# Kernel optimization log

Measured on AMD Instinct MI355X. Metric: run time of the kernel, lower is better.

Reference implementation:

```python
import jax, jax.numpy as jnp
import numpy as np

NEG_INF = -1e9
ALPHA = 0.2  # LeakyReLU slope


def gat_layer(x, adj, W, a_src, a_dst):
    # x: (N, F), adj: (N, N) bool, W: (F, H, D), a_src/a_dst: (H, D)
    h = jnp.einsum('nf,fhd->nhd', x, W)                 # (N, H, D)
    es = jnp.einsum('nhd,hd->nh', h, a_src)             # score from target node i
    ed = jnp.einsum('nhd,hd->nh', h, a_dst)             # score from neighbor j
    e = jax.nn.leaky_relu(es[:, None, :] + ed[None, :, :], ALPHA)  # (N, N, H)
    e = jnp.where(adj[:, :, None], e, NEG_INF)
    attn = jax.nn.softmax(e, axis=1)                    # softmax over neighbors j
    out = jnp.einsum('ijh,jhd->ihd', attn, h)           # (N, H, D)
    N, H, D = out.shape
    return out.reshape(N, H * D)                        # concat heads


def setup_inputs() -> dict:
    key = jax.random.key(0)
    ks = jax.random.split(key, 8)
    N, F, H1, D1, C = 4096, 512, 8, 8, 16
    node_matrix = jax.random.normal(ks[0], (N, F), dtype=jnp.float32)
    adj = jax.random.bernoulli(ks[1], 0.005, (N, N))
    adj = jnp.logical_or(adj, jnp.eye(N, dtype=bool))   # self-loops
    s1 = 1.0 / np.sqrt(F)
    s2 = 1.0 / np.sqrt(H1 * D1)
    return {
        'node_matrix': node_matrix,
        'adj_matrix': adj,
        'W1': jax.random.normal(ks[2], (F, H1, D1), dtype=jnp.float32) * s1,
        'a1_src': jax.random.normal(ks[3], (H1, D1), dtype=jnp.float32) * s1,
        'a1_dst': jax.random.normal(ks[4], (H1, D1), dtype=jnp.float32) * s1,
        'W2': jax.random.normal(ks[5], (H1 * D1, 1, C), dtype=jnp.float32) * s2,
        'a2_src': jax.random.normal(ks[6], (1, C), dtype=jnp.float32) * s2,
        'a2_dst': jax.random.normal(ks[7], (1, C), dtype=jnp.float32) * s2,
    }


def reference(node_matrix, adj_matrix, W1, a1_src, a1_dst, W2, a2_src, a2_dst):
    # dropout layers are identity in eval mode
    z1 = gat_layer(node_matrix, adj_matrix, W1, a1_src, a1_dst)  # (N, 64)
    a1 = jax.nn.elu(z1)
    z2 = gat_layer(a1, adj_matrix, W2, a2_src, a2_dst)           # (N, num_classes)
    return z2
```

## Files before the change

### kernel.cpp

```cpp
#include <hip/hip_runtime.h>

#define N_NODES 4096
#define F_IN    512
#define NH1     8
#define F1      64
#define C2      16
#define MAXDEG  128

__device__ __forceinline__ float wave_sum(float v) {
    for (int o = 32; o >= 1; o >>= 1) v += __shfl_xor(v, o, 64);
    return v;
}

__global__ void detect_width_kernel(const unsigned char* __restrict__ adj,
                                    int* __restrict__ flag) {
    __shared__ unsigned int cnts[4];
    __shared__ unsigned int mxv;
    int t = threadIdx.x;
    if (t < 4) cnts[t] = 0u;
    if (t == 0) mxv = 0u;
    __syncthreads();
    unsigned int c0 = 0, c1 = 0, c2 = 0, c3 = 0, m = 0;
    const unsigned int* p = (const unsigned int*)(adj) + t * 64;
    for (int i = 0; i < 64; ++i) {
        unsigned int v = p[i];
        unsigned int b0 = v & 0xffu, b1 = (v >> 8) & 0xffu;
        unsigned int b2 = (v >> 16) & 0xffu, b3 = (v >> 24) & 0xffu;
        if (b0) { c0++; m = m > b0 ? m : b0; }
        if (b1) { c1++; m = m > b1 ? m : b1; }
        if (b2) { c2++; m = m > b2 ? m : b2; }
        if (b3) { c3++; m = m > b3 ? m : b3; }
    }
    atomicAdd(&cnts[0], c0); atomicAdd(&cnts[1], c1);
    atomicAdd(&cnts[2], c2); atomicAdd(&cnts[3], c3);
    atomicMax(&mxv, m);
    __syncthreads();
    if (t == 0) {
        int w;
        if (cnts[1] + cnts[2] + cnts[3] == 0u)      w = 4;
        else if (cnts[0] == 0u && cnts[1] == 0u)    w = 4;
        else if (cnts[0] == 0u && cnts[2] == 0u)    w = 2;
        else if (mxv <= 1u)                          w = 1;
        else                                         w = 2;
        *flag = w;
    }
}

__global__ __launch_bounds__(256) void frontend_kernel(
        const unsigned char* __restrict__ adj, const int* __restrict__ flag,
        unsigned short* __restrict__ neigh, int* __restrict__ deg,
        const float* __restrict__ x, const float* __restrict__ W1,
        const float* __restrict__ asrc, const float* __restrict__ adst,
        float* __restrict__ h1, float* __restrict__ es, float* __restrict__ ed) {
    __shared__ __align__(16) char smem[24576];
    const int t = threadIdx.x;

    if (blockIdx.x < N_NODES) {
        int* cnt = (int*)smem;
        const int row = blockIdx.x;
        if (t == 0) *cnt = 0;
        __syncthreads();
        const int w = *flag;
        unsigned short* outp = neigh + (size_t)row * MAXDEG;
        if (w == 1) {
            const uint4* p = (const uint4*)(adj + (size_t)row * N_NODES);
            uint4 v = p[t];
            if (v.x | v.y | v.z | v.w) {
                unsigned int wd[4] = {v.x, v.y, v.z, v.w};
                int base = t * 16;
                for (int q = 0; q < 4; ++q) {
                    unsigned int word = wd[q];
                    for (int bb = 0; bb < 4; ++bb) {
                        if ((word >> (8 * bb)) & 0xffu) {
                            int pos = atomicAdd(cnt, 1);
                            if (pos < MAXDEG) outp[pos] = (unsigned short)(base + q * 4 + bb);
                        }
                    }
                }
            }
        } else if (w == 2) {
            const uint4* p = (const uint4*)(adj + (size_t)row * N_NODES * 2);
            uint4 v[2];
            #pragma unroll
            for (int i = 0; i < 2; ++i) v[i] = p[t + i * 256];
            #pragma unroll
            for (int i = 0; i < 2; ++i) {
                if ((v[i].x | v[i].y | v[i].z | v[i].w) == 0u) continue;
                unsigned int wd[4] = {v[i].x, v[i].y, v[i].z, v[i].w};
                int base = (t + i * 256) * 8;
                for (int q = 0; q < 4; ++q) {
                    unsigned int word = wd[q];
                    if (word & 0xffffu) {
                        int pos = atomicAdd(cnt, 1);
                        if (pos < MAXDEG) outp[pos] = (unsigned short)(base + q * 2);
                    }
                    if (word >> 16) {
                        int pos = atomicAdd(cnt, 1);
                        if (pos < MAXDEG) outp[pos] = (unsigned short)(base + q * 2 + 1);
                    }
                }
            }
        } else {
            const uint4* p = (const uint4*)(adj + (size_t)row * N_NODES * 4);
            uint4 v[4];
            #pragma unroll
            for (int i = 0; i < 4; ++i) v[i] = p[t + i * 256];
            #pragma unroll
            for (int i = 0; i < 4; ++i) {
                if ((v[i].x | v[i].y | v[i].z | v[i].w) == 0u) continue;
                unsigned int wd[4] = {v[i].x, v[i].y, v[i].z, v[i].w};
                int base = (t + i * 256) * 4;
                for (int q = 0; q < 4; ++q) {
                    if (wd[q]) {
                        int pos = atomicAdd(cnt, 1);
                        if (pos < MAXDEG) outp[pos] = (unsigned short)(base + q);
                    }
                }
            }
        }
        __syncthreads();
        if (t == 0) deg[row] = min(*cnt, MAXDEG);
    } else {
        float* xs = (float*)smem;
        float* wt = (float*)(smem + 8192);
        const int row0 = (blockIdx.x - N_NODES) * 4;
        const float4* src = (const float4*)(x + (size_t)row0 * F_IN);
        float4* dst = (float4*)xs;
        for (int i = t; i < 4 * F_IN / 4; i += 256) dst[i] = src[i];
        const int c = t & 63;
        const int r = t >> 6;
        const float4* w1v = (const float4*)W1;
        float4* wtv = (float4*)wt;
        float a = 0.f;
        for (int k0 = 0; k0 < F_IN; k0 += 64) {
            __syncthreads();
            #pragma unroll
            for (int i = 0; i < 4; ++i)
                wtv[t + i * 256] = w1v[k0 * 16 + t + i * 256];
            __syncthreads();
            const float4* xr = (const float4*)&xs[r * F_IN + k0];
            #pragma unroll
            for (int kk = 0; kk < 64; kk += 4) {
                float4 xv = xr[kk >> 2];
                float w0 = wt[(kk + 0) * 64 + c];
                float w1 = wt[(kk + 1) * 64 + c];
                float w2 = wt[(kk + 2) * 64 + c];
                float w3 = wt[(kk + 3) * 64 + c];
                a += xv.x * w0 + xv.y * w1 + xv.z * w2 + xv.w * w3;
            }
        }
        const int n = row0 + r;
        h1[(size_t)n * F1 + c] = a;
        float s = a * asrc[c];
        float d = a * adst[c];
        s += __shfl_xor(s, 1); s += __shfl_xor(s, 2); s += __shfl_xor(s, 4);
        d += __shfl_xor(d, 1); d += __shfl_xor(d, 2); d += __shfl_xor(d, 4);
        if ((c & 7) == 0) {
            es[n * NH1 + (c >> 3)] = s;
            ed[n * NH1 + (c >> 3)] = d;
        }
    }
}

__global__ __launch_bounds__(256) void attn1_kernel(
        const unsigned short* __restrict__ neigh, const int* __restrict__ deg,
        const float* __restrict__ h1, const float* __restrict__ es,
        const float* __restrict__ ed, const float* __restrict__ W2,
        const float* __restrict__ a2s, const float* __restrict__ a2d,
        float* __restrict__ h2, float* __restrict__ es2, float* __restrict__ ed2) {
    __shared__ unsigned short listA[4 * MAXDEG];
    __shared__ float arowA[4 * 64];
    __shared__ float pbufA[4 * 576];
    const int t = threadIdx.x;
    const int wv = t >> 6;
    const int l = t & 63;
    const int i = blockIdx.x * 4 + wv;
    unsigned short* list = listA + wv * MAXDEG;
    float* arow = arowA + wv * 64;
    float* pw   = pbufA + wv * 576;
    const int hq = l >> 3;

    const int K = deg[i];
    const unsigned short* lst = neigh + (size_t)i * MAXDEG;
    for (int j = l; j < MAXDEG; j += 64) list[j] = (j < K) ? lst[j] : (unsigned short)0;
    __syncthreads();

    float plsum[NH1], esi[NH1];
    #pragma unroll
    for (int h = 0; h < NH1; ++h) plsum[h] = 0.f;
    #pragma unroll
    for (int h = 0; h < NH1; ++h) esi[h] = es[i * NH1 + h];
    float acc = 0.f;

    for (int t0 = 0; t0 < MAXDEG; t0 += 64) {
        const int tc = min(64, K - t0);
        if (tc > 0) {
            const bool valid = l < tc;
            const int j = valid ? (int)list[t0 + l] : 0;
            #pragma unroll
            for (int h = 0; h < NH1; ++h) {
                float v = esi[h] + ed[j * NH1 + h];
                v = (v >= 0.f) ? v : 0.2f * v;
                float p = valid ? __expf(v) : 0.f;
                plsum[h] += p;
                pw[l * 9 + h] = p;
            }
        }
        __syncthreads();
        if (tc > 0) {
            const int tcPad = (tc + 7) & ~7;
            for (int u = 0; u < tcPad; u += 8) {
                #pragma unroll
                for (int vv = 0; vv < 8; ++vv) {
                    int jn = (int)list[t0 + u + vv];
                    acc += pw[(u + vv) * 9 + hq] * h1[(size_t)jn * F1 + l];
                }
            }
        }
        __syncthreads();
    }
    float lsum[NH1];
    #pragma unroll
    for (int h = 0; h < NH1; ++h) lsum[h] = wave_sum(plsum[h]);
    float o = acc / lsum[hq];
    float a1v = (o > 0.f) ? o : (__expf(o) - 1.f);

    arow[l] = a1v;
    __syncthreads();
    const int cc = l & 15;
    const int kg = l >> 4;
    float hacc = 0.f;
    #pragma unroll
    for (int k = 0; k < 16; ++k)
        hacc += arow[kg * 16 + k] * W2[(kg * 16 + k) * C2 + cc];
    hacc += __shfl_xor(hacc, 16);
    hacc += __shfl_xor(hacc, 32);
    if (l < C2) h2[(size_t)i * C2 + l] = hacc;
    float s2 = hacc * a2s[cc];
    float d2 = hacc * a2d[cc];
    s2 += __shfl_xor(s2, 1); s2 += __shfl_xor(s2, 2);
    s2 += __shfl_xor(s2, 4); s2 += __shfl_xor(s2, 8);
    d2 += __shfl_xor(d2, 1); d2 += __shfl_xor(d2, 2);
    d2 += __shfl_xor(d2, 4); d2 += __shfl_xor(d2, 8);
    if (l == 0) { es2[i] = s2; ed2[i] = d2; }
}

__global__ __launch_bounds__(256) void attn2_kernel(
        const unsigned short* __restrict__ neigh, const int* __restrict__ deg,
        const float* __restrict__ h2, const float* __restrict__ es2,
        const float* __restrict__ ed2, float* __restrict__ out) {
    __shared__ unsigned short listA[4 * MAXDEG];
    __shared__ float pbufA[4 * 64];
    const int t = threadIdx.x;
    const int wv = t >> 6;
    const int l = t & 63;
    const int i = blockIdx.x * 4 + wv;
    unsigned short* list = listA + wv * MAXDEG;
    float* pb = pbufA + wv * 64;
    const int c = l & 15;
    const int g = l >> 4;

    const int K = deg[i];
    const unsigned short* lst = neigh + (size_t)i * MAXDEG;
    for (int j = l; j < MAXDEG; j += 64) list[j] = (j < K) ? lst[j] : (unsigned short)0;
    __syncthreads();

    float plsum = 0.f, acc = 0.f;
    const float esi = es2[i];
    for (int t0 = 0; t0 < MAXDEG; t0 += 64) {
        const int tc = min(64, K - t0);
        if (tc > 0) {
            const bool valid = l < tc;
            const int j = valid ? (int)list[t0 + l] : 0;
            float v = esi + ed2[j];
            v = (v >= 0.f) ? v : 0.2f * v;
            float p = valid ? __expf(v) : 0.f;
            plsum += p;
            pb[l] = p;
        }
        __syncthreads();
        if (tc > 0) {
            const int tcPad = (tc + 3) & ~3;
            for (int u = g; u < tcPad; u += 4) {
                int jn = (int)list[t0 + u];
                acc += pb[u] * h2[(size_t)jn * C2 + c];
            }
        }
        __syncthreads();
    }
    float lsum = wave_sum(plsum);
    acc += __shfl_xor(acc, 16);
    acc += __shfl_xor(acc, 32);
    if (l < C2) out[(size_t)i * C2 + l] = acc / lsum;
}

extern "C" void kernel_launch(void* const* d_in, const int* in_sizes, int n_in,
                              void* d_out, int out_size, void* d_ws, size_t ws_size,
                              hipStream_t stream) {
    const float* x           = (const float*)d_in[0];
    const unsigned char* adj = (const unsigned char*)d_in[1];
    const float* W1          = (const float*)d_in[2];
    const float* a1src       = (const float*)d_in[3];
    const float* a1dst       = (const float*)d_in[4];
    const float* W2          = (const float*)d_in[5];
    const float* a2src       = (const float*)d_in[6];
    const float* a2dst       = (const float*)d_in[7];
    float* out = (float*)d_out;

    char* ws = (char*)d_ws;
    size_t off = 0;
    int* flag = (int*)(ws + off);                 off += 256;
    unsigned short* neigh = (unsigned short*)(ws + off);
    off += (size_t)N_NODES * MAXDEG * 2;
    int* deg = (int*)(ws + off);                  off += (size_t)N_NODES * 4;
    float* h1 = (float*)(ws + off);               off += (size_t)N_NODES * F1 * 4;
    float* es1 = (float*)(ws + off);              off += (size_t)N_NODES * NH1 * 4;
    float* ed1 = (float*)(ws + off);              off += (size_t)N_NODES * NH1 * 4;
    float* h2 = (float*)(ws + off);               off += (size_t)N_NODES * C2 * 4;
    float* es2 = (float*)(ws + off);              off += (size_t)N_NODES * 4;
    float* ed2 = (float*)(ws + off);              off += (size_t)N_NODES * 4;

    hipLaunchKernelGGL(detect_width_kernel, dim3(1), dim3(256), 0, stream, adj, flag);
    hipLaunchKernelGGL(frontend_kernel, dim3(N_NODES + N_NODES / 4), dim3(256), 0, stream,
                       adj, flag, neigh, deg, x, W1, a1src, a1dst, h1, es1, ed1);
    hipLaunchKernelGGL(attn1_kernel, dim3(N_NODES / 4), dim3(256), 0, stream,
                       neigh, deg, h1, es1, ed1, W2, a2src, a2dst, h2, es2, ed2);
    hipLaunchKernelGGL(attn2_kernel, dim3(N_NODES / 4), dim3(256), 0, stream,
                       neigh, deg, h2, es2, ed2, out);
}
```

Measured before the change: 158.4 us.

## Restructure frontend GEMM with 8-row double-buffered tiles and per-wave adjacency scan

The W1 projection now computes 8 rows per block, reusing each loaded W1 tile across twice as many rows and prefetching the next tile into a second shared buffer. Adjacency scanning moves from one row per 256-thread block to one row per wavefront, with each lane loading several uint4s. The attention kernels swap block-wide syncthreads for wave barriers, since each wave works on its own data, and their neighbor loops now stop at the real degree. The detect kernel reads uint4 vectors. Together these aim to cut W1 reloads, block count and sync overhead, at the cost of more registers and LDS per block.

```diff
diff --git a/kernel.cpp b/kernel.cpp
--- a/kernel.cpp
+++ b/kernel.cpp
@@ -6,6 +6,9 @@
 #define F1      64
 #define C2      16
 #define MAXDEG  128
+
+#define GEMM_BLKS (N_NODES / 8)
+#define SCAN_BLKS (N_NODES / 4)
 
 __device__ __forceinline__ float wave_sum(float v) {
     for (int o = 32; o >= 1; o >>= 1) v += __shfl_xor(v, o, 64);
@@ -21,15 +24,21 @@
     if (t == 0) mxv = 0u;
     __syncthreads();
     unsigned int c0 = 0, c1 = 0, c2 = 0, c3 = 0, m = 0;
-    const unsigned int* p = (const unsigned int*)(adj) + t * 64;
-    for (int i = 0; i < 64; ++i) {
-        unsigned int v = p[i];
-        unsigned int b0 = v & 0xffu, b1 = (v >> 8) & 0xffu;
-        unsigned int b2 = (v >> 16) & 0xffu, b3 = (v >> 24) & 0xffu;
-        if (b0) { c0++; m = m > b0 ? m : b0; }
-        if (b1) { c1++; m = m > b1 ? m : b1; }
-        if (b2) { c2++; m = m > b2 ? m : b2; }
-        if (b3) { c3++; m = m > b3 ? m : b3; }
+    const uint4* p = (const uint4*)(adj) + t * 16;
+    #pragma unroll
+    for (int i = 0; i < 16; ++i) {
+        uint4 q = p[i];
+        unsigned int wd[4] = {q.x, q.y, q.z, q.w};
+        #pragma unroll
+        for (int k = 0; k < 4; ++k) {
+            unsigned int v = wd[k];
+            unsigned int b0 = v & 0xffu, b1 = (v >> 8) & 0xffu;
+            unsigned int b2 = (v >> 16) & 0xffu, b3 = (v >> 24) & 0xffu;
+            if (b0) { c0++; m = m > b0 ? m : b0; }
+            if (b1) { c1++; m = m > b1 ? m : b1; }
+            if (b2) { c2++; m = m > b2 ? m : b2; }
+            if (b3) { c3++; m = m > b3 ? m : b3; }
+        }
     }
     atomicAdd(&cnts[0], c0); atomicAdd(&cnts[1], c1);
     atomicAdd(&cnts[2], c2); atomicAdd(&cnts[3], c3);
@@ -52,22 +61,94 @@
         const float* __restrict__ x, const float* __restrict__ W1,
         const float* __restrict__ asrc, const float* __restrict__ adst,
         float* __restrict__ h1, float* __restrict__ es, float* __restrict__ ed) {
-    __shared__ __align__(16) char smem[24576];
+    __shared__ __align__(16) float smem[4096 + 2 * 4096];
+    __shared__ int scnt[4];
     const int t = threadIdx.x;
-
-    if (blockIdx.x < N_NODES) {
-        int* cnt = (int*)smem;
-        const int row = blockIdx.x;
-        if (t == 0) *cnt = 0;
-        __syncthreads();
+    const int wv = t >> 6;
+    const int l = t & 63;
+
+    if (blockIdx.x < GEMM_BLKS) {
+        float* xs  = smem;
+        float* wt0 = smem + 4096;
+        float* wt1 = smem + 8192;
+        const int row0 = blockIdx.x * 8;
+
+        {
+            const float4* src = (const float4*)(x + (size_t)row0 * F_IN);
+            float4* dst = (float4*)xs;
+            #pragma unroll
+            for (int i = 0; i < 4; ++i) dst[t + i * 256] = src[t + i * 256];
+        }
+        const float4* w1v = (const float4*)W1;
+        {
+            float4* d = (float4*)wt0;
+            #pragma unroll
+            for (int i = 0; i < 4; ++i) d[t + i * 256] = w1v[t + i * 256];
+        }
+
+        const int c = t & 63;
+        const int rq = t >> 6;
+        float a0 = 0.f, a1 = 0.f;
+        float* wcur = wt0;
+        float* wnxt = wt1;
+        for (int tile = 0; tile < 8; ++tile) {
+            __syncthreads();
+            float4 pf0, pf1, pf2, pf3;
+            if (tile < 7) {
+                const float4* s = w1v + (size_t)(tile + 1) * 1024;
+                pf0 = s[t]; pf1 = s[t + 256]; pf2 = s[t + 512]; pf3 = s[t + 768];
+            }
+            const float4* xr0 = (const float4*)&xs[rq * F_IN + tile * 64];
+            const float4* xr1 = (const float4*)&xs[(rq + 4) * F_IN + tile * 64];
+            #pragma unroll
+            for (int kk = 0; kk < 64; kk += 4) {
+                float4 x0 = xr0[kk >> 2];
+                float4 x1 = xr1[kk >> 2];
+                float w0 = wcur[(kk + 0) * 64 + c];
+                float w1 = wcur[(kk + 1) * 64 + c];
+                float w2 = wcur[(kk + 2) * 64 + c];
+                float w3 = wcur[(kk + 3) * 64 + c];
+                a0 += x0.x * w0 + x0.y * w1 + x0.z * w2 + x0.w * w3;
+                a1 += x1.x * w0 + x1.y * w1 + x1.z * w2 + x1.w * w3;
+            }
+            if (tile < 7) {
+                float4* d = (float4*)wnxt;
+                d[t] = pf0; d[t + 256] = pf1; d[t + 512] = pf2; d[t + 768] = pf3;
+            }
+            float* tmp = wcur; wcur = wnxt; wnxt = tmp;
+        }
+
+        const int n0 = row0 + rq;
+        h1[(size_t)n0 * F1 + c] = a0;
+        h1[(size_t)(n0 + 4) * F1 + c] = a1;
+        float s0 = a0 * asrc[c], d0 = a0 * adst[c];
+        float s1 = a1 * asrc[c], d1 = a1 * adst[c];
+        s0 += __shfl_xor(s0, 1); s0 += __shfl_xor(s0, 2); s0 += __shfl_xor(s0, 4);
+        d0 += __shfl_xor(d0, 1); d0 += __shfl_xor(d0, 2); d0 += __shfl_xor(d0, 4);
+        s1 += __shfl_xor(s1, 1); s1 += __shfl_xor(s1, 2); s1 += __shfl_xor(s1, 4);
+        d1 += __shfl_xor(d1, 1); d1 += __shfl_xor(d1, 2); d1 += __shfl_xor(d1, 4);
+        if ((c & 7) == 0) {
+            es[n0 * NH1 + (c >> 3)] = s0;
+            ed[n0 * NH1 + (c >> 3)] = d0;
+            es[(n0 + 4) * NH1 + (c >> 3)] = s1;
+            ed[(n0 + 4) * NH1 + (c >> 3)] = d1;
+        }
+    } else {
+        const int row = (blockIdx.x - GEMM_BLKS) * 4 + wv;
+        int* cnt = scnt + wv;
+        if (l == 0) *cnt = 0;
         const int w = *flag;
         unsigned short* outp = neigh + (size_t)row * MAXDEG;
         if (w == 1) {
             const uint4* p = (const uint4*)(adj + (size_t)row * N_NODES);
-            uint4 v = p[t];
-            if (v.x | v.y | v.z | v.w) {
-                unsigned int wd[4] = {v.x, v.y, v.z, v.w};
-                int base = t * 16;
+            uint4 v[4];
+            #pragma unroll
+            for (int i = 0; i < 4; ++i) v[i] = p[l + 64 * i];
+            #pragma unroll
+            for (int i = 0; i < 4; ++i) {
+                if ((v[i].x | v[i].y | v[i].z | v[i].w) == 0u) continue;
+                unsigned int wd[4] = {v[i].x, v[i].y, v[i].z, v[i].w};
+                int base = (l + 64 * i) * 16;
                 for (int q = 0; q < 4; ++q) {
                     unsigned int word = wd[q];
                     for (int bb = 0; bb < 4; ++bb) {
@@ -80,14 +161,14 @@
             }
         } else if (w == 2) {
             const uint4* p = (const uint4*)(adj + (size_t)row * N_NODES * 2);
-            uint4 v[2];
-            #pragma unroll
-            for (int i = 0; i < 2; ++i) v[i] = p[t + i * 256];
-            #pragma unroll
-            for (int i = 0; i < 2; ++i) {
+            uint4 v[8];
+            #pragma unroll
+            for (int i = 0; i < 8; ++i) v[i] = p[l + 64 * i];
+            #pragma unroll
+            for (int i = 0; i < 8; ++i) {
                 if ((v[i].x | v[i].y | v[i].z | v[i].w) == 0u) continue;
                 unsigned int wd[4] = {v[i].x, v[i].y, v[i].z, v[i].w};
-                int base = (t + i * 256) * 8;
+                int base = (l + 64 * i) * 8;
                 for (int q = 0; q < 4; ++q) {
                     unsigned int word = wd[q];
                     if (word & 0xffffu) {
@@ -102,63 +183,26 @@
             }
         } else {
             const uint4* p = (const uint4*)(adj + (size_t)row * N_NODES * 4);
-            uint4 v[4];
-            #pragma unroll
-            for (int i = 0; i < 4; ++i) v[i] = p[t + i * 256];
-            #pragma unroll
-            for (int i = 0; i < 4; ++i) {
-                if ((v[i].x | v[i].y | v[i].z | v[i].w) == 0u) continue;
-                unsigned int wd[4] = {v[i].x, v[i].y, v[i].z, v[i].w};
-                int base = (t + i * 256) * 4;
-                for (int q = 0; q < 4; ++q) {
-                    if (wd[q]) {
-                        int pos = atomicAdd(cnt, 1);
-                        if (pos < MAXDEG) outp[pos] = (unsigned short)(base + q);
+            #pragma unroll
+            for (int b = 0; b < 2; ++b) {
+                uint4 v[8];
+                #pragma unroll
+                for (int i = 0; i < 8; ++i) v[i] = p[l + 64 * (b * 8 + i)];
+                #pragma unroll
+                for (int i = 0; i < 8; ++i) {
+                    if ((v[i].x | v[i].y | v[i].z | v[i].w) == 0u) continue;
+                    unsigned int wd[4] = {v[i].x, v[i].y, v[i].z, v[i].w};
+                    int base = (l + 64 * (b * 8 + i)) * 4;
+                    for (int q = 0; q < 4; ++q) {
+                        if (wd[q]) {
+                            int pos = atomicAdd(cnt, 1);
+                            if (pos < MAXDEG) outp[pos] = (unsigned short)(base + q);
+                        }
                     }
                 }
             }
         }
-        __syncthreads();
-        if (t == 0) deg[row] = min(*cnt, MAXDEG);
-    } else {
-        float* xs = (float*)smem;
-        float* wt = (float*)(smem + 8192);
-        const int row0 = (blockIdx.x - N_NODES) * 4;
-        const float4* src = (const float4*)(x + (size_t)row0 * F_IN);
-        float4* dst = (float4*)xs;
-        for (int i = t; i < 4 * F_IN / 4; i += 256) dst[i] = src[i];
-        const int c = t & 63;
-        const int r = t >> 6;
-        const float4* w1v = (const float4*)W1;
-        float4* wtv = (float4*)wt;
-        float a = 0.f;
-        for (int k0 = 0; k0 < F_IN; k0 += 64) {
-            __syncthreads();
-            #pragma unroll
-            for (int i = 0; i < 4; ++i)
-                wtv[t + i * 256] = w1v[k0 * 16 + t + i * 256];
-            __syncthreads();
-            const float4* xr = (const float4*)&xs[r * F_IN + k0];
-            #pragma unroll
-            for (int kk = 0; kk < 64; kk += 4) {
-                float4 xv = xr[kk >> 2];
-                float w0 = wt[(kk + 0) * 64 + c];
-                float w1 = wt[(kk + 1) * 64 + c];
-                float w2 = wt[(kk + 2) * 64 + c];
-                float w3 = wt[(kk + 3) * 64 + c];
-                a += xv.x * w0 + xv.y * w1 + xv.z * w2 + xv.w * w3;
-            }
-        }
-        const int n = row0 + r;
-        h1[(size_t)n * F1 + c] = a;
-        float s = a * asrc[c];
-        float d = a * adst[c];
-        s += __shfl_xor(s, 1); s += __shfl_xor(s, 2); s += __shfl_xor(s, 4);
-        d += __shfl_xor(d, 1); d += __shfl_xor(d, 2); d += __shfl_xor(d, 4);
-        if ((c & 7) == 0) {
-            es[n * NH1 + (c >> 3)] = s;
-            ed[n * NH1 + (c >> 3)] = d;
-        }
+        if (l == 0) deg[row] = min(*cnt, MAXDEG);
     }
 }
 
@@ -183,41 +227,41 @@
     const int K = deg[i];
     const unsigned short* lst = neigh + (size_t)i * MAXDEG;
     for (int j = l; j < MAXDEG; j += 64) list[j] = (j < K) ? lst[j] : (unsigned short)0;
-    __syncthreads();
-
-    float plsum[NH1], esi[NH1];
+    __builtin_amdgcn_wave_barrier();
+
+    float plsum[NH1];
     #pragma unroll
     for (int h = 0; h < NH1; ++h) plsum[h] = 0.f;
-    #pragma unroll
-    for (int h = 0; h < NH1; ++h) esi[h] = es[i * NH1 + h];
+    const float4 e0 = *(const float4*)(es + (size_t)i * NH1);
+    const float4 e1 = *(const float4*)(es + (size_t)i * NH1 + 4);
+    const float esi[NH1] = {e0.x, e0.y, e0.z, e0.w, e1.x, e1.y, e1.z, e1.w};
     float acc = 0.f;
 
-    for (int t0 = 0; t0 < MAXDEG; t0 += 64) {
+    for (int t0 = 0; t0 < K; t0 += 64) {
         const int tc = min(64, K - t0);
-        if (tc > 0) {
-            const bool valid = l < tc;
-            const int j = valid ? (int)list[t0 + l] : 0;
-            #pragma unroll
-            for (int h = 0; h < NH1; ++h) {
-                float v = esi[h] + ed[j * NH1 + h];
-                v = (v >= 0.f) ? v : 0.2f * v;
-                float p = valid ? __expf(v) : 0.f;
-                plsum[h] += p;
-                pw[l * 9 + h] = p;
-            }
-        }
-        __syncthreads();
-        if (tc > 0) {
-            const int tcPad = (tc + 7) & ~7;
-            for (int u = 0; u < tcPad; u += 8) {
-                #pragma unroll
-                for (int vv = 0; vv < 8; ++vv) {
-                    int jn = (int)list[t0 + u + vv];
-                    acc += pw[(u + vv) * 9 + hq] * h1[(size_t)jn * F1 + l];
-                }
-            }
-        }
-        __syncthreads();
+        const bool valid = l < tc;
+        const int j = valid ? (int)list[t0 + l] : 0;
+        const float4 d0 = *(const float4*)(ed + (size_t)j * NH1);
+        const float4 d1 = *(const float4*)(ed + (size_t)j * NH1 + 4);
+        const float edv[NH1] = {d0.x, d0.y, d0.z, d0.w, d1.x, d1.y, d1.z, d1.w};
+        #pragma unroll
+        for (int h = 0; h < NH1; ++h) {
+            float v = esi[h] + edv[h];
+            v = (v >= 0.f) ? v : 0.2f * v;
+            float p = valid ? __expf(v) : 0.f;
+            plsum[h] += p;
+            pw[l * 9 + h] = p;
+        }
+        __builtin_amdgcn_wave_barrier();
+        const int tcPad = (tc + 7) & ~7;
+        for (int u = 0; u < tcPad; u += 8) {
+            #pragma unroll
+            for (int vv = 0; vv < 8; ++vv) {
+                int jn = (int)list[t0 + u + vv];
+                acc += pw[(u + vv) * 9 + hq] * h1[(size_t)jn * F1 + l];
+            }
+        }
+        __builtin_amdgcn_wave_barrier();
     }
     float lsum[NH1];
     #pragma unroll
@@ -226,7 +270,7 @@
     float a1v = (o > 0.f) ? o : (__expf(o) - 1.f);
 
     arow[l] = a1v;
-    __syncthreads();
+    __builtin_amdgcn_wave_barrier();
     const int cc = l & 15;
     const int kg = l >> 4;
     float hacc = 0.f;
@@ -263,30 +307,26 @@
     const int K = deg[i];
     const unsigned short* lst = neigh + (size_t)i * MAXDEG;
     for (int j = l; j < MAXDEG; j += 64) list[j] = (j < K) ? lst[j] : (unsigned short)0;
-    __syncthreads();
+    __builtin_amdgcn_wave_barrier();
 
     float plsum = 0.f, acc = 0.f;
     const float esi = es2[i];
-    for (int t0 = 0; t0 < MAXDEG; t0 += 64) {
+    for (int t0 = 0; t0 < K; t0 += 64) {
         const int tc = min(64, K - t0);
-        if (tc > 0) {
-            const bool valid = l < tc;
-            const int j = valid ? (int)list[t0 + l] : 0;
-            float v = esi + ed2[j];
-            v = (v >= 0.f) ? v : 0.2f * v;
-            float p = valid ? __expf(v) : 0.f;
-            plsum += p;
-            pb[l] = p;
-        }
-        __syncthreads();
-        if (tc > 0) {
-            const int tcPad = (tc + 3) & ~3;
-            for (int u = g; u < tcPad; u += 4) {
-                int jn = (int)list[t0 + u];
-                acc += pb[u] * h2[(size_t)jn * C2 + c];
-            }
-        }
-        __syncthreads();
+        const bool valid = l < tc;
+        const int j = valid ? (int)list[t0 + l] : 0;
+        float v = esi + ed2[j];
+        v = (v >= 0.f) ? v : 0.2f * v;
+        float p = valid ? __expf(v) : 0.f;
+        plsum += p;
+        pb[l] = p;
+        __builtin_amdgcn_wave_barrier();
+        const int tcPad = (tc + 3) & ~3;
+        for (int u = g; u < tcPad; u += 4) {
+            int jn = (int)list[t0 + u];
+            acc += pb[u] * h2[(size_t)jn * C2 + c];
+        }
+        __builtin_amdgcn_wave_barrier();
     }
     float lsum = wave_sum(plsum);
     acc += __shfl_xor(acc, 16);
@@ -321,7 +361,7 @@
     float* ed2 = (float*)(ws + off);              off += (size_t)N_NODES * 4;
 
     hipLaunchKernelGGL(detect_width_kernel, dim3(1), dim3(256), 0, stream, adj, flag);
-    hipLaunchKernelGGL(frontend_kernel, dim3(N_NODES + N_NODES / 4), dim3(256), 0, stream,
+    hipLaunchKernelGGL(frontend_kernel, dim3(GEMM_BLKS + SCAN_BLKS), dim3(256), 0, stream,
                        adj, flag, neigh, deg, x, W1, a1src, a1dst, h1, es1, ed1);
     hipLaunchKernelGGL(attn1_kernel, dim3(N_NODES / 4), dim3(256), 0, stream,
                        neigh, deg, h1, es1, ed1, W2, a2src, a2dst, h2, es2, ed2);
```

After: 145.9 us. -7.8%, faster.
